# Performance work log

Measured on AMD Instinct MI355X. Metric: run time of the kernel, lower is better.

The kernel has to match this reference:

```python
import jax, jax.numpy as jnp
import numpy as np

HIDDEN = 2048
HEADS = 16
HEAD_DIM = HIDDEN // HEADS  # 128
ROPE_BASE = 10000.0


def _rope_cos_sin(seq_len, head_dim, dtype):
    inv_freq = 1.0 / (ROPE_BASE ** (jnp.arange(0, head_dim, 2, dtype=jnp.float32) / head_dim))
    pos = jnp.arange(seq_len, dtype=jnp.float32)
    freqs = pos[:, None] * inv_freq[None, :]            # [S, D/2]
    emb = jnp.concatenate([freqs, freqs], axis=-1)      # [S, D]
    return jnp.cos(emb).astype(dtype), jnp.sin(emb).astype(dtype)


def _rotate_half(x):
    x1, x2 = jnp.split(x, 2, axis=-1)
    return jnp.concatenate([-x2, x1], axis=-1)


def apply_rope(q, k, seq_len):
    # q, k: [B, H, S, Dh]
    cos, sin = _rope_cos_sin(seq_len, q.shape[-1], q.dtype)
    q = q * cos + _rotate_half(q) * sin
    k = k * cos + _rotate_half(k) * sin
    return q, k


def setup_inputs() -> dict:
    key = jax.random.key(0)
    ks = jax.random.split(key, 5)
    B, S = 2, 2048
    scale = 1.0 / np.sqrt(HIDDEN)
    return {
        "hidden_states": jax.random.normal(ks[0], (B, S, HIDDEN), dtype=jnp.float32),
        "w_qkv": jax.random.normal(ks[1], (3 * HIDDEN, HIDDEN), dtype=jnp.float32) * scale,
        "b_qkv": jnp.zeros((3 * HIDDEN,), dtype=jnp.float32),
        "w_dense": jax.random.normal(ks[2], (HIDDEN, HIDDEN), dtype=jnp.float32) * scale,
        "b_dense": jnp.zeros((HIDDEN,), dtype=jnp.float32),
    }


def reference(hidden_states, w_qkv, b_qkv, w_dense, b_dense):
    B, S, _ = hidden_states.shape
    qkv = hidden_states @ w_qkv.T + b_qkv                      # [B, S, 3*H*Dh]
    qkv = qkv.reshape(B, S, 3, HEADS, HEAD_DIM)
    qkv = jnp.transpose(qkv, (2, 0, 3, 1, 4))                  # [3, B, H, S, Dh]
    q, k, v = qkv[0], qkv[1], qkv[2]

    # pos_encoding.apply_to_qk -> RoPE
    q, k = apply_rope(q, k, S)

    scale = HEAD_DIM ** (-0.5)
    scores = jnp.einsum("bhqd,bhkd->bhqk", q, k) * scale       # [B, H, S, S]

    # pos_encoding.apply_to_scores -> causal additive mask
    causal = jnp.tril(jnp.ones((S, S), dtype=bool))
    scores = jnp.where(causal, scores, jnp.finfo(scores.dtype).min)

    attn = jax.nn.softmax(scores, axis=-1)
    out = jnp.einsum("bhqk,bhkd->bhqd", attn, v)               # [B, H, S, Dh]
    out = jnp.transpose(out, (0, 2, 1, 3)).reshape(B, S, HIDDEN)
    return out @ w_dense.T + b_dense
```

## Files before the change

### kernel.cpp

```cpp
#include <hip/hip_runtime.h>
#include <hip/hip_bf16.h>
#include <stdint.h>

#define HID 2048
#define NHEAD 16
#define DHEAD 128
#define BB 2
#define SS 2048
#define MM (BB*SS)
#define NQKV (3*HID)
#define NT (SS/64)

typedef __attribute__((ext_vector_type(8))) short bf16x8;
typedef __attribute__((ext_vector_type(4))) float f32x4;
typedef unsigned short ushort_t;

__device__ __forceinline__ f32x4 mfma16(bf16x8 a, bf16x8 b, f32x4 c) {
    return __builtin_amdgcn_mfma_f32_16x16x32_bf16(a, b, c, 0, 0, 0);
}

__device__ __forceinline__ float bf2f(ushort_t u) {
    unsigned int x = ((unsigned int)u) << 16;
    return __builtin_bit_cast(float, x);
}
__device__ __forceinline__ ushort_t f2bf(float f) {
    unsigned int x = __builtin_bit_cast(unsigned int, f);
    unsigned int r = (x + 0x7FFFu + ((x >> 16) & 1u)) >> 16;
    return (ushort_t)r;
}

__device__ __forceinline__ void cvt8(const float* __restrict__ g, ushort_t* l) {
    float4 a = *(const float4*)g;
    float4 b = *(const float4*)(g + 4);
    union { ushort_t u[8]; uint4 v; } t;
    t.u[0] = f2bf(a.x); t.u[1] = f2bf(a.y); t.u[2] = f2bf(a.z); t.u[3] = f2bf(a.w);
    t.u[4] = f2bf(b.x); t.u[5] = f2bf(b.y); t.u[6] = f2bf(b.z); t.u[7] = f2bf(b.w);
    *(uint4*)l = t.v;
}

__device__ __forceinline__ void gload16(const ushort_t* g, ushort_t* l) {
    __builtin_amdgcn_global_load_lds(
        (const __attribute__((address_space(1))) unsigned int*)(const void*)g,
        (__attribute__((address_space(3))) unsigned int*)(void*)l,
        16, 0, 0);
}

__global__ void cvt3_kernel(const float* __restrict__ a, ushort_t* __restrict__ da, int na,
                            const float* __restrict__ b, ushort_t* __restrict__ db, int nb,
                            const float* __restrict__ c, ushort_t* __restrict__ dc, int nc)
{
    int i = blockIdx.x * blockDim.x + threadIdx.x;
    if (i < na) {
        cvt8(a + (size_t)i * 8, da + (size_t)i * 8);
    } else if (i < na + nb) {
        int j = i - na;
        cvt8(b + (size_t)j * 8, db + (size_t)j * 8);
    } else if (i < na + nb + nc) {
        int j = i - na - nb;
        cvt8(c + (size_t)j * 8, dc + (size_t)j * 8);
    }
}

__global__ __launch_bounds__(256, 2) void qkv_gemm_fast(
    const ushort_t* __restrict__ X,
    const ushort_t* __restrict__ W,
    const float* __restrict__ bias,
    ushort_t* __restrict__ qws,
    ushort_t* __restrict__ kws,
    ushort_t* __restrict__ vtws)
{
    __shared__ __align__(16) ushort_t As[128 * 32];
    __shared__ __align__(16) ushort_t Bs[128 * 32];
    const int tid  = threadIdx.x;
    const int lane = tid & 63;
    const int w    = tid >> 6;
    const int wm   = w >> 1, wn = w & 1;
    const int quad = lane >> 4;
    const int l15  = lane & 15;
    const int m0 = blockIdx.y * 128;
    const int n0 = blockIdx.x * 128;
    const bool vmode = (n0 >= 2 * HID);

    f32x4 acc[4][4];
    for (int i = 0; i < 4; i++)
        for (int j = 0; j < 4; j++)
            for (int e = 0; e < 4; e++) acc[i][j][e] = 0.f;

    for (int k0 = 0; k0 < HID; k0 += 32) {
        __syncthreads();
#pragma unroll
        for (int i = 0; i < 2; i++) {
            int cbase = i * 256 + w * 64;
            int c = cbase + lane;
            int row = c >> 2, cc = c & 3;
            gload16(X + (size_t)(m0 + row) * HID + k0 + cc * 8, As + cbase * 8);
            gload16(W + (size_t)(n0 + row) * HID + k0 + cc * 8, Bs + cbase * 8);
        }
        __syncthreads();

        bf16x8 afr[4], bfr[4];
#pragma unroll
        for (int mb = 0; mb < 4; mb++)
            afr[mb] = *(const bf16x8*)(As + (wm * 64 + mb * 16 + l15) * 32 + quad * 8);
#pragma unroll
        for (int nb = 0; nb < 4; nb++)
            bfr[nb] = *(const bf16x8*)(Bs + (wn * 64 + nb * 16 + l15) * 32 + quad * 8);
        if (!vmode) {
#pragma unroll
            for (int mb = 0; mb < 4; mb++)
#pragma unroll
                for (int nb = 0; nb < 4; nb++)
                    acc[mb][nb] = mfma16(afr[mb], bfr[nb], acc[mb][nb]);
        } else {
#pragma unroll
            for (int mb = 0; mb < 4; mb++)
#pragma unroll
                for (int nb = 0; nb < 4; nb++)
                    acc[mb][nb] = mfma16(bfr[nb], afr[mb], acc[mb][nb]);
        }
    }

    if (!vmode) {
#pragma unroll
        for (int nb = 0; nb < 4; nb++) {
            int n = n0 + wn * 64 + nb * 16 + l15;
            float bv = bias[n];
            int mat = n >> 11;
            int h   = (n >> 7) & 15;
            int d   = n & 127;
            ushort_t* dst = (mat == 0) ? qws : kws;
#pragma unroll
            for (int mb = 0; mb < 4; mb++) {
#pragma unroll
                for (int r = 0; r < 4; r++) {
                    int m = m0 + wm * 64 + mb * 16 + quad * 4 + r;
                    int b = m >> 11;
                    int s = m & 2047;
                    dst[(((size_t)(b * 16 + h) * SS) + s) * DHEAD + d] =
                        f2bf(acc[mb][nb][r] + bv);
                }
            }
        }
    } else {
        const int b = m0 >> 11;
#pragma unroll
        for (int nb = 0; nb < 4; nb++) {
#pragma unroll
            for (int r = 0; r < 4; r++) {
                int n = n0 + wn * 64 + nb * 16 + quad * 4 + r;
                float bv = bias[n];
                int h = (n >> 7) & 15;
                int d = n & 127;
#pragma unroll
                for (int mb = 0; mb < 4; mb++) {
                    int s = (m0 & 2047) + wm * 64 + mb * 16 + l15;
                    vtws[(((size_t)(b * 16 + h) * DHEAD) + d) * SS + s] =
                        f2bf(acc[mb][nb][r] + bv);
                }
            }
        }
    }
}

__global__ __launch_bounds__(256, 2) void dense_gemm_fast(
    const ushort_t* __restrict__ A,
    const ushort_t* __restrict__ W,
    const float* __restrict__ bias,
    float* __restrict__ out)
{
    __shared__ __align__(16) ushort_t As[128 * 32];
    __shared__ __align__(16) ushort_t Bs[128 * 32];
    const int tid  = threadIdx.x;
    const int lane = tid & 63;
    const int w    = tid >> 6;
    const int wm   = w >> 1, wn = w & 1;
    const int quad = lane >> 4;
    const int l15  = lane & 15;
    const int m0 = blockIdx.y * 128;
    const int n0 = blockIdx.x * 128;

    f32x4 acc[4][4];
    for (int i = 0; i < 4; i++)
        for (int j = 0; j < 4; j++)
            for (int e = 0; e < 4; e++) acc[i][j][e] = 0.f;

    for (int k0 = 0; k0 < HID; k0 += 32) {
        __syncthreads();
#pragma unroll
        for (int i = 0; i < 2; i++) {
            int cbase = i * 256 + w * 64;
            int c = cbase + lane;
            int row = c >> 2, cc = c & 3;
            gload16(A + (size_t)(m0 + row) * HID + k0 + cc * 8, As + cbase * 8);
            gload16(W + (size_t)(n0 + row) * HID + k0 + cc * 8, Bs + cbase * 8);
        }
        __syncthreads();

        bf16x8 afr[4], bfr[4];
#pragma unroll
        for (int mb = 0; mb < 4; mb++)
            afr[mb] = *(const bf16x8*)(As + (wm * 64 + mb * 16 + l15) * 32 + quad * 8);
#pragma unroll
        for (int nb = 0; nb < 4; nb++)
            bfr[nb] = *(const bf16x8*)(Bs + (wn * 64 + nb * 16 + l15) * 32 + quad * 8);
#pragma unroll
        for (int mb = 0; mb < 4; mb++)
#pragma unroll
            for (int nb = 0; nb < 4; nb++)
                acc[mb][nb] = mfma16(afr[mb], bfr[nb], acc[mb][nb]);
    }

#pragma unroll
    for (int nb = 0; nb < 4; nb++) {
        int n = n0 + wn * 64 + nb * 16 + l15;
        float bv = bias[n];
#pragma unroll
        for (int mb = 0; mb < 4; mb++) {
#pragma unroll
            for (int r = 0; r < 4; r++) {
                int m = m0 + wm * 64 + mb * 16 + quad * 4 + r;
                out[(size_t)m * HID + n] = acc[mb][nb][r] + bv;
            }
        }
    }
}

__global__ void rope_kernel2(ushort_t* __restrict__ qws, ushort_t* __restrict__ kws)
{
    int idx = blockIdx.x * blockDim.x + threadIdx.x;
    int d2 = idx & 63;
    int s  = idx >> 6;

    float inv_freq = exp2f(-(float)d2 * (13.287712379549449f / 64.f));
    float fr = (float)s * inv_freq;
    float sn, cs;
    sincosf(fr, &sn, &cs);

    size_t base0 = (size_t)s * DHEAD + d2;
#pragma unroll
    for (int bh = 0; bh < BB * NHEAD; bh++) {
        size_t base = base0 + (size_t)bh * (SS * DHEAD);
        float q1 = bf2f(qws[base]);
        float q2 = bf2f(qws[base + 64]);
        qws[base]      = f2bf(q1 * cs - q2 * sn);
        qws[base + 64] = f2bf(q2 * cs + q1 * sn);
        float k1 = bf2f(kws[base]);
        float k2 = bf2f(kws[base + 64]);
        kws[base]      = f2bf(k1 * cs - k2 * sn);
        kws[base + 64] = f2bf(k2 * cs + k1 * sn);
    }
}

#define LDP 72

__global__ __launch_bounds__(256, 2) void attn_kernel4(
    const ushort_t* __restrict__ qws,
    const ushort_t* __restrict__ kws,
    const ushort_t* __restrict__ vtws,
    ushort_t* __restrict__ aout)
{
    __shared__ __align__(16) ushort_t k_s[64 * 128];
    __shared__ __align__(16) ushort_t vt_s[128 * 64];
    __shared__ __align__(16) ushort_t pA_s[4][16 * LDP];
    __shared__ __align__(16) ushort_t pB_s[4][16 * LDP];

    const int tid  = threadIdx.x;
    const int lane = tid & 63;
    const int w    = tid >> 6;
    const int quad = lane >> 4;
    const int l15  = lane & 15;

    const int g  = blockIdx.x;
    const int bh = (g & 7) | (((g >> 3) & 3) << 3);
    const int tA = g >> 5;
    const int tB = NT - 1 - tA;
    const int qA = tA * 64, qB = tB * 64;
    const size_t qk_base = (size_t)bh * SS * DHEAD;

    bf16x8 qa[4], qb[4];
    {
        const ushort_t* rowA = qws + qk_base + (size_t)(qA + w * 16 + l15) * DHEAD;
        const ushort_t* rowB = qws + qk_base + (size_t)(qB + w * 16 + l15) * DHEAD;
#pragma unroll
        for (int kc = 0; kc < 4; kc++) {
            qa[kc] = *(const bf16x8*)(rowA + kc * 32 + quad * 8);
            qb[kc] = *(const bf16x8*)(rowB + kc * 32 + quad * 8);
        }
    }

    bf16x8 ones;
#pragma unroll
    for (int i = 0; i < 8; i++) ones[i] = (short)0x3F80;

    f32x4 oA[8], oB[8], lA, lB;
#pragma unroll
    for (int i = 0; i < 8; i++)
#pragma unroll
        for (int e = 0; e < 4; e++) { oA[i][e] = 0.f; oB[i][e] = 0.f; }
#pragma unroll
    for (int e = 0; e < 4; e++) { lA[e] = 0.f; lB[e] = 0.f; }

    const int srowK = lane >> 4;
    const int srowV = lane >> 3;
    const int ccgV  = (lane & 7) ^ (lane >> 3);

    const int q_baseA = qA + w * 16 + quad * 4;
    const int q_baseB = qB + w * 16 + quad * 4;
    const int xorv = l15 & 7;

    const float scale2 = 0.12753102015727466f;
    const float FM = 16.0f;

    for (int j = 0; j <= tB; j++) {
        const int kb = j * 64;
        __syncthreads();
#pragma unroll
        for (int i = 0; i < 4; i++) {
            int P = i * 4 + w;
            int row = P * 4 + srowK;
            int ccg = l15 ^ (((P & 1) * 4) + srowK);
            gload16(kws + qk_base + (size_t)(kb + row) * DHEAD + ccg * 8,
                    k_s + P * 512);
        }
#pragma unroll
        for (int i = 0; i < 4; i++) {
            int P = i * 4 + w;
            int row = P * 8 + srowV;
            gload16(vtws + qk_base + (size_t)row * SS + kb + ccgV * 8,
                    vt_s + P * 512);
        }
        __syncthreads();

        f32x4 sA[4], sB[4];
#pragma unroll
        for (int nb = 0; nb < 4; nb++)
#pragma unroll
            for (int e = 0; e < 4; e++) { sA[nb][e] = 0.f; sB[nb][e] = 0.f; }

        if (j <= tA) {
#pragma unroll
            for (int kc = 0; kc < 4; kc++) {
#pragma unroll
                for (int nb = 0; nb < 4; nb++) {
                    int cc_s = (kc * 4 + quad) ^ xorv;
                    bf16x8 kf = *(const bf16x8*)(k_s + (nb * 16 + l15) * 128 + cc_s * 8);
                    sA[nb] = mfma16(qa[kc], kf, sA[nb]);
                    sB[nb] = mfma16(qb[kc], kf, sB[nb]);
                }
            }
#pragma unroll
            for (int nb = 0; nb < 4; nb++) {
                int kidx = kb + nb * 16 + l15;
#pragma unroll
                for (int r = 0; r < 4; r++) {
                    float pa = exp2f(sA[nb][r] * scale2 - FM);
                    float pb = exp2f(sB[nb][r] * scale2 - FM);
                    pa = (kidx <= q_baseA + r) ? pa : 0.f;
                    pb = (kidx <= q_baseB + r) ? pb : 0.f;
                    pA_s[w][(quad * 4 + r) * LDP + nb * 16 + l15] = f2bf(pa);
                    pB_s[w][(quad * 4 + r) * LDP + nb * 16 + l15] = f2bf(pb);
                }
            }
#pragma unroll
            for (int kc = 0; kc < 2; kc++) {
                bf16x8 pa = *(const bf16x8*)(pA_s[w] + l15 * LDP + kc * 32 + quad * 8);
                bf16x8 pb = *(const bf16x8*)(pB_s[w] + l15 * LDP + kc * 32 + quad * 8);
                lA = mfma16(pa, ones, lA);
                lB = mfma16(pb, ones, lB);
#pragma unroll
                for (int db = 0; db < 8; db++) {
                    int cc_s = (kc * 4 + quad) ^ xorv;
                    bf16x8 vf = *(const bf16x8*)(vt_s + (db * 16 + l15) * 64 + cc_s * 8);
                    oA[db] = mfma16(pa, vf, oA[db]);
                    oB[db] = mfma16(pb, vf, oB[db]);
                }
            }
        } else {
#pragma unroll
            for (int kc = 0; kc < 4; kc++) {
#pragma unroll
                for (int nb = 0; nb < 4; nb++) {
                    int cc_s = (kc * 4 + quad) ^ xorv;
                    bf16x8 kf = *(const bf16x8*)(k_s + (nb * 16 + l15) * 128 + cc_s * 8);
                    sB[nb] = mfma16(qb[kc], kf, sB[nb]);
                }
            }
#pragma unroll
            for (int nb = 0; nb < 4; nb++) {
                int kidx = kb + nb * 16 + l15;
#pragma unroll
                for (int r = 0; r < 4; r++) {
                    float pb = exp2f(sB[nb][r] * scale2 - FM);
                    pb = (kidx <= q_baseB + r) ? pb : 0.f;
                    pB_s[w][(quad * 4 + r) * LDP + nb * 16 + l15] = f2bf(pb);
                }
            }
#pragma unroll
            for (int kc = 0; kc < 2; kc++) {
                bf16x8 pb = *(const bf16x8*)(pB_s[w] + l15 * LDP + kc * 32 + quad * 8);
                lB = mfma16(pb, ones, lB);
#pragma unroll
                for (int db = 0; db < 8; db++) {
                    int cc_s = (kc * 4 + quad) ^ xorv;
                    bf16x8 vf = *(const bf16x8*)(vt_s + (db * 16 + l15) * 64 + cc_s * 8);
                    oB[db] = mfma16(pb, vf, oB[db]);
                }
            }
        }
    }

    const int b = bh >> 4;
    const int h = bh & 15;
    float invA[4], invB[4];
#pragma unroll
    for (int r = 0; r < 4; r++) { invA[r] = 1.f / lA[r]; invB[r] = 1.f / lB[r]; }
#pragma unroll
    for (int db = 0; db < 8; db++) {
#pragma unroll
        for (int r = 0; r < 4; r++) {
            int sA_row = qA + w * 16 + quad * 4 + r;
            int sB_row = qB + w * 16 + quad * 4 + r;
            size_t offA = ((size_t)(b * SS + sA_row)) * HID + h * DHEAD + db * 16 + l15;
            size_t offB = ((size_t)(b * SS + sB_row)) * HID + h * DHEAD + db * 16 + l15;
            aout[offA] = f2bf(oA[db][r] * invA[r]);
            aout[offB] = f2bf(oB[db][r] * invB[r]);
        }
    }
}

extern "C" void kernel_launch(void* const* d_in, const int* in_sizes, int n_in,
                              void* d_out, int out_size, void* d_ws, size_t ws_size,
                              hipStream_t stream)
{
    const float* X    = (const float*)d_in[0];
    const float* Wqkv = (const float*)d_in[1];
    const float* bqkv = (const float*)d_in[2];
    const float* Wd   = (const float*)d_in[3];
    const float* bd   = (const float*)d_in[4];
    float* out = (float*)d_out;

    char* ws = (char*)d_ws;
    const size_t MB = 1048576;
    ushort_t* qws  = (ushort_t*)(ws);
    ushort_t* kws  = (ushort_t*)(ws + 16 * MB);
    ushort_t* vtws = (ushort_t*)(ws + 32 * MB);
    ushort_t* aout = (ushort_t*)(ws + 48 * MB);
    ushort_t* Xbf  = (ushort_t*)(ws + 48 * MB);
    ushort_t* Wqbf = (ushort_t*)(ws + 64 * MB);
    ushort_t* Wdbf = (ushort_t*)(ws + 88 * MB);

    const int nX = MM * HID / 8, nWq = NQKV * HID / 8, nWd = HID * HID / 8;
    cvt3_kernel<<<(nX + nWq + nWd + 255) / 256, 256, 0, stream>>>(
        X, Xbf, nX, Wqkv, Wqbf, nWq, Wd, Wdbf, nWd);

    qkv_gemm_fast<<<dim3(NQKV / 128, MM / 128), 256, 0, stream>>>(Xbf, Wqbf, bqkv, qws, kws, vtws);
    rope_kernel2<<<(SS * 64) / 256, 256, 0, stream>>>(qws, kws);
    attn_kernel4<<<dim3(NT / 2 * BB * NHEAD), 256, 0, stream>>>(qws, kws, vtws, aout);
    dense_gemm_fast<<<dim3(HID / 128, MM / 128), 256, 0, stream>>>(aout, Wdbf, bd, out);
}
```

Before: 410.5 us.

## Triple-buffer QKV and dense GEMMs with swizzled LDS and 256x128 tiles

Both projection GEMMs move to 512-thread blocks with 256x128 output tiles and a K step of 64. A three-stage LDS ring is filled by async global-to-LDS loads, with vmcnt waits and raw barriers replacing the two syncthreads per iteration. LDS rows are XOR-swizzled to avoid bank conflicts, and setprio raises wave priority around the MFMA block. The aim is to overlap global loads with matrix math and cut barrier overhead, at the cost of more LDS (144KB per block), one block per CU, and fewer blocks for the dense GEMM.

```diff
diff --git a/kernel.cpp b/kernel.cpp
--- a/kernel.cpp
+++ b/kernel.cpp
@@ -61,7 +61,15 @@
     }
 }
 
-__global__ __launch_bounds__(256, 2) void qkv_gemm_fast(
+#define BM 256
+#define BN 128
+#define BKK 64
+#define NTK (HID/BKK)
+#define ASZ (BM*BKK)
+#define BSZ (BN*BKK)
+#define BUFSZ (ASZ+BSZ)
+
+__global__ __launch_bounds__(512, 1) void qkv_gemm_fast(
     const ushort_t* __restrict__ X,
     const ushort_t* __restrict__ W,
     const float* __restrict__ bias,
@@ -69,56 +77,103 @@
     ushort_t* __restrict__ kws,
     ushort_t* __restrict__ vtws)
 {
-    __shared__ __align__(16) ushort_t As[128 * 32];
-    __shared__ __align__(16) ushort_t Bs[128 * 32];
+    __shared__ __align__(16) ushort_t smem[3 * BUFSZ];
+
     const int tid  = threadIdx.x;
     const int lane = tid & 63;
     const int w    = tid >> 6;
-    const int wm   = w >> 1, wn = w & 1;
+    const int wm   = w >> 1;
+    const int wn   = w & 1;
     const int quad = lane >> 4;
     const int l15  = lane & 15;
-    const int m0 = blockIdx.y * 128;
-    const int n0 = blockIdx.x * 128;
+    const int sub  = (lane & 7) ^ (lane >> 3);
+    const int rloc = lane >> 3;
+    const int m0 = blockIdx.y * BM;
+    const int n0 = blockIdx.x * BN;
     const bool vmode = (n0 >= 2 * HID);
 
+    const ushort_t* gA = X + (size_t)m0 * HID;
+    const ushort_t* gB = W + (size_t)n0 * HID;
+
     f32x4 acc[4][4];
+#pragma unroll
     for (int i = 0; i < 4; i++)
+#pragma unroll
         for (int j = 0; j < 4; j++)
+#pragma unroll
             for (int e = 0; e < 4; e++) acc[i][j][e] = 0.f;
 
-    for (int k0 = 0; k0 < HID; k0 += 32) {
-        __syncthreads();
+    auto STAGE = [&](int bufi, int t) {
+        ushort_t* lA = smem + bufi * BUFSZ;
+        ushort_t* lB = lA + ASZ;
+        const ushort_t* ga = gA + t * BKK;
+        const ushort_t* gb = gB + t * BKK;
+#pragma unroll
+        for (int i = 0; i < 4; i++) {
+            int blk = w * 4 + i;
+            gload16(ga + (size_t)(blk * 8 + rloc) * HID + sub * 8, lA + blk * 512);
+        }
 #pragma unroll
         for (int i = 0; i < 2; i++) {
-            int cbase = i * 256 + w * 64;
-            int c = cbase + lane;
-            int row = c >> 2, cc = c & 3;
-            gload16(X + (size_t)(m0 + row) * HID + k0 + cc * 8, As + cbase * 8);
-            gload16(W + (size_t)(n0 + row) * HID + k0 + cc * 8, Bs + cbase * 8);
-        }
-        __syncthreads();
-
-        bf16x8 afr[4], bfr[4];
-#pragma unroll
-        for (int mb = 0; mb < 4; mb++)
-            afr[mb] = *(const bf16x8*)(As + (wm * 64 + mb * 16 + l15) * 32 + quad * 8);
-#pragma unroll
-        for (int nb = 0; nb < 4; nb++)
-            bfr[nb] = *(const bf16x8*)(Bs + (wn * 64 + nb * 16 + l15) * 32 + quad * 8);
+            int blk = w * 2 + i;
+            gload16(gb + (size_t)(blk * 8 + rloc) * HID + sub * 8, lB + blk * 512);
+        }
+    };
+
+    auto COMPUTE = [&](int bufi) {
+        const ushort_t* lA = smem + bufi * BUFSZ;
+        const ushort_t* lB = lA + ASZ;
+        bf16x8 af[2][4], bfr[2][4];
+#pragma unroll
+        for (int kk = 0; kk < 2; kk++) {
+            const int cs = ((kk * 4 + quad) ^ (l15 & 7)) << 3;
+#pragma unroll
+            for (int mb = 0; mb < 4; mb++)
+                af[kk][mb] = *(const bf16x8*)(lA + (wm * 64 + mb * 16 + l15) * 64 + cs);
+#pragma unroll
+            for (int nb = 0; nb < 4; nb++)
+                bfr[kk][nb] = *(const bf16x8*)(lB + (wn * 64 + nb * 16 + l15) * 64 + cs);
+        }
+        __builtin_amdgcn_s_setprio(1);
         if (!vmode) {
 #pragma unroll
-            for (int mb = 0; mb < 4; mb++)
-#pragma unroll
-                for (int nb = 0; nb < 4; nb++)
-                    acc[mb][nb] = mfma16(afr[mb], bfr[nb], acc[mb][nb]);
+            for (int kk = 0; kk < 2; kk++)
+#pragma unroll
+                for (int mb = 0; mb < 4; mb++)
+#pragma unroll
+                    for (int nb = 0; nb < 4; nb++)
+                        acc[mb][nb] = mfma16(af[kk][mb], bfr[kk][nb], acc[mb][nb]);
         } else {
 #pragma unroll
-            for (int mb = 0; mb < 4; mb++)
-#pragma unroll
-                for (int nb = 0; nb < 4; nb++)
-                    acc[mb][nb] = mfma16(bfr[nb], afr[mb], acc[mb][nb]);
-        }
-    }
+            for (int kk = 0; kk < 2; kk++)
+#pragma unroll
+                for (int mb = 0; mb < 4; mb++)
+#pragma unroll
+                    for (int nb = 0; nb < 4; nb++)
+                        acc[mb][nb] = mfma16(bfr[kk][nb], af[kk][mb], acc[mb][nb]);
+        }
+        __builtin_amdgcn_s_setprio(0);
+    };
+
+    STAGE(0, 0);
+    STAGE(1, 1);
+    asm volatile("s_waitcnt vmcnt(6)" ::: "memory");
+    __builtin_amdgcn_s_barrier();
+
+    int buf = 0;
+    for (int t = 0; t < NTK - 2; t++) {
+        int b2 = buf + 2; if (b2 >= 3) b2 -= 3;
+        STAGE(b2, t + 2);
+        COMPUTE(buf);
+        asm volatile("s_waitcnt vmcnt(6)" ::: "memory");
+        __builtin_amdgcn_s_barrier();
+        buf++; if (buf == 3) buf = 0;
+    }
+    COMPUTE(buf);
+    asm volatile("s_waitcnt vmcnt(0)" ::: "memory");
+    __builtin_amdgcn_s_barrier();
+    buf++; if (buf == 3) buf = 0;
+    COMPUTE(buf);
 
     if (!vmode) {
 #pragma unroll
@@ -162,53 +217,98 @@
     }
 }
 
-__global__ __launch_bounds__(256, 2) void dense_gemm_fast(
+__global__ __launch_bounds__(512, 1) void dense_gemm_fast(
     const ushort_t* __restrict__ A,
     const ushort_t* __restrict__ W,
     const float* __restrict__ bias,
     float* __restrict__ out)
 {
-    __shared__ __align__(16) ushort_t As[128 * 32];
-    __shared__ __align__(16) ushort_t Bs[128 * 32];
+    __shared__ __align__(16) ushort_t smem[3 * BUFSZ];
+
     const int tid  = threadIdx.x;
     const int lane = tid & 63;
     const int w    = tid >> 6;
-    const int wm   = w >> 1, wn = w & 1;
+    const int wm   = w >> 1;
+    const int wn   = w & 1;
     const int quad = lane >> 4;
     const int l15  = lane & 15;
-    const int m0 = blockIdx.y * 128;
-    const int n0 = blockIdx.x * 128;
+    const int sub  = (lane & 7) ^ (lane >> 3);
+    const int rloc = lane >> 3;
+    const int m0 = blockIdx.y * BM;
+    const int n0 = blockIdx.x * BN;
+
+    const ushort_t* gA = A + (size_t)m0 * HID;
+    const ushort_t* gB = W + (size_t)n0 * HID;
 
     f32x4 acc[4][4];
+#pragma unroll
     for (int i = 0; i < 4; i++)
+#pragma unroll
         for (int j = 0; j < 4; j++)
+#pragma unroll
             for (int e = 0; e < 4; e++) acc[i][j][e] = 0.f;
 
-    for (int k0 = 0; k0 < HID; k0 += 32) {
-        __syncthreads();
+    auto STAGE = [&](int bufi, int t) {
+        ushort_t* lA = smem + bufi * BUFSZ;
+        ushort_t* lB = lA + ASZ;
+        const ushort_t* ga = gA + t * BKK;
+        const ushort_t* gb = gB + t * BKK;
+#pragma unroll
+        for (int i = 0; i < 4; i++) {
+            int blk = w * 4 + i;
+            gload16(ga + (size_t)(blk * 8 + rloc) * HID + sub * 8, lA + blk * 512);
+        }
 #pragma unroll
         for (int i = 0; i < 2; i++) {
-            int cbase = i * 256 + w * 64;
-            int c = cbase + lane;
-            int row = c >> 2, cc = c & 3;
-            gload16(A + (size_t)(m0 + row) * HID + k0 + cc * 8, As + cbase * 8);
-            gload16(W + (size_t)(n0 + row) * HID + k0 + cc * 8, Bs + cbase * 8);
-        }
-        __syncthreads();
-
-        bf16x8 afr[4], bfr[4];
-#pragma unroll
-        for (int mb = 0; mb < 4; mb++)
-            afr[mb] = *(const bf16x8*)(As + (wm * 64 + mb * 16 + l15) * 32 + quad * 8);
-#pragma unroll
-        for (int nb = 0; nb < 4; nb++)
-            bfr[nb] = *(const bf16x8*)(Bs + (wn * 64 + nb * 16 + l15) * 32 + quad * 8);
-#pragma unroll
-        for (int mb = 0; mb < 4; mb++)
+            int blk = w * 2 + i;
+            gload16(gb + (size_t)(blk * 8 + rloc) * HID + sub * 8, lB + blk * 512);
+        }
+    };
+
+    auto COMPUTE = [&](int bufi) {
+        const ushort_t* lA = smem + bufi * BUFSZ;
+        const ushort_t* lB = lA + ASZ;
+        bf16x8 af[2][4], bfr[2][4];
+#pragma unroll
+        for (int kk = 0; kk < 2; kk++) {
+            const int cs = ((kk * 4 + quad) ^ (l15 & 7)) << 3;
+#pragma unroll
+            for (int mb = 0; mb < 4; mb++)
+                af[kk][mb] = *(const bf16x8*)(lA + (wm * 64 + mb * 16 + l15) * 64 + cs);
 #pragma unroll
             for (int nb = 0; nb < 4; nb++)
-                acc[mb][nb] = mfma16(afr[mb], bfr[nb], acc[mb][nb]);
-    }
+                bfr[kk][nb] = *(const bf16x8*)(lB + (wn * 64 + nb * 16 + l15) * 64 + cs);
+        }
+        __builtin_amdgcn_s_setprio(1);
+#pragma unroll
+        for (int kk = 0; kk < 2; kk++)
+#pragma unroll
+            for (int mb = 0; mb < 4; mb++)
+#pragma unroll
+                for (int nb = 0; nb < 4; nb++)
+                    acc[mb][nb] = mfma16(af[kk][mb], bfr[kk][nb], acc[mb][nb]);
+        __builtin_amdgcn_s_setprio(0);
+    };
+
+    STAGE(0, 0);
+    STAGE(1, 1);
+    asm volatile("s_waitcnt vmcnt(6)" ::: "memory");
+    __builtin_amdgcn_s_barrier();
+
+    int buf = 0;
+    for (int t = 0; t < NTK - 2; t++) {
+        int b2 = buf + 2; if (b2 >= 3) b2 -= 3;
+        STAGE(b2, t + 2);
+        COMPUTE(buf);
+        asm volatile("s_waitcnt vmcnt(6)" ::: "memory");
+        __builtin_amdgcn_s_barrier();
+        buf++; if (buf == 3) buf = 0;
+    }
+    COMPUTE(buf);
+    asm volatile("s_waitcnt vmcnt(0)" ::: "memory");
+    __builtin_amdgcn_s_barrier();
+    buf++; if (buf == 3) buf = 0;
+    COMPUTE(buf);
 
 #pragma unroll
     for (int nb = 0; nb < 4; nb++) {
@@ -453,8 +553,8 @@
     cvt3_kernel<<<(nX + nWq + nWd + 255) / 256, 256, 0, stream>>>(
         X, Xbf, nX, Wqkv, Wqbf, nWq, Wd, Wdbf, nWd);
 
-    qkv_gemm_fast<<<dim3(NQKV / 128, MM / 128), 256, 0, stream>>>(Xbf, Wqbf, bqkv, qws, kws, vtws);
+    qkv_gemm_fast<<<dim3(NQKV / BN, MM / BM), 512, 0, stream>>>(Xbf, Wqbf, bqkv, qws, kws, vtws);
     rope_kernel2<<<(SS * 64) / 256, 256, 0, stream>>>(qws, kws);
     attn_kernel4<<<dim3(NT / 2 * BB * NHEAD), 256, 0, stream>>>(qws, kws, vtws, aout);
-    dense_gemm_fast<<<dim3(HID / 128, MM / 128), 256, 0, stream>>>(aout, Wdbf, bd, out);
-}
+    dense_gemm_fast<<<dim3(HID / BN, MM / BM), 512, 0, stream>>>(aout, Wdbf, bd, out);
+}
```

Result: faster. 376.2 us (-8.4%).
